# Optimization experiments

Measured on AMD Instinct MI355X. Metric: run time of the kernel, lower is better.

The kernel has to match this reference:

```python
import jax, jax.numpy as jnp
import numpy as np

NUM_HEADS = 16
HEAD_DIM = 64
LN_EPS = 1e-12


def _interleave_pairs(a, b):
    # stack([a, b], -1).reshape(..., 2*d) -> interleaved on last dim
    return jnp.stack([a, b], axis=-1).reshape(a.shape[:-1] + (a.shape[-1] * 2,))


def _rotate_half(x):
    # stack([-x[..., 1::2], x[..., ::2]], -1).reshape_as(x)
    return _interleave_pairs(-x[..., 1::2], x[..., ::2])


def setup_inputs() -> dict:
    key = jax.random.key(0)
    ks = jax.random.split(key, 4)
    B, S, H = 4, 2048, 1024
    hidden_states = jax.random.normal(ks[0], (B, S, H), dtype=jnp.float32)
    sinusoidal_pos = jax.random.uniform(ks[1], (1, 1, S, HEAD_DIM), dtype=jnp.float32)
    ln_weight = jnp.ones((H,), dtype=jnp.float32)
    ln_bias = jnp.zeros((H,), dtype=jnp.float32)
    w_qkv = jax.random.normal(ks[2], (H, 3 * H), dtype=jnp.float32) * (1.0 / np.sqrt(H))
    b_qkv = jax.random.normal(ks[3], (3 * H,), dtype=jnp.float32) * 0.02
    return {"hidden_states": hidden_states, "sinusoidal_pos": sinusoidal_pos,
            "ln_weight": ln_weight, "ln_bias": ln_bias, "w_qkv": w_qkv, "b_qkv": b_qkv}


def reference(hidden_states, sinusoidal_pos, ln_weight, ln_bias, w_qkv, b_qkv):
    B, S, H = hidden_states.shape
    # LayerNorm
    mu = jnp.mean(hidden_states, axis=-1, keepdims=True)
    var = jnp.mean(jnp.square(hidden_states - mu), axis=-1, keepdims=True)
    h = (hidden_states - mu) * jax.lax.rsqrt(var + LN_EPS) * ln_weight + ln_bias
    # Fused QKV projection
    qkv = h @ w_qkv + b_qkv                       # [B, S, 3H]
    q, k, v = jnp.split(qkv, 3, axis=-1)
    def to_heads(x):
        return x.reshape(B, S, NUM_HEADS, HEAD_DIM).transpose(0, 2, 1, 3)  # [B, Hn, S, D]
    q, k, v = to_heads(q), to_heads(k), to_heads(v)
    # RoPE (RoFormer interleaved style)
    sin, cos = jnp.split(sinusoidal_pos, 2, axis=-1)      # each [1,1,S,D/2]
    sin_pos = _interleave_pairs(sin, sin)                 # [1,1,S,D]
    cos_pos = _interleave_pairs(cos, cos)
    q = q * cos_pos + _rotate_half(q) * sin_pos
    k = k * cos_pos + _rotate_half(k) * sin_pos
    # SDPA (non-causal, no mask, eval-mode dropout=0)
    scale = 1.0 / np.sqrt(HEAD_DIM)
    scores = jnp.einsum('bhqd,bhkd->bhqk', q, k) * scale
    probs = jax.nn.softmax(scores, axis=-1)
    ctx = jnp.einsum('bhqk,bhkd->bhqd', probs, v)         # [B, Hn, S, D]
    ctx = ctx.transpose(0, 2, 1, 3).reshape(B, S, H)
    return ctx
```

## Files before the change

kernel.cpp:

```cpp
#include <hip/hip_runtime.h>
#include <hip/hip_bf16.h>
#include <cstdint>
#include <cstddef>

#define DEVINL __device__ __forceinline__

typedef float f32x4 __attribute__((ext_vector_type(4)));
typedef float f32x16 __attribute__((ext_vector_type(16)));
typedef short s16x8 __attribute__((ext_vector_type(8)));
typedef short s16x4 __attribute__((ext_vector_type(4)));

static constexpr int Sd = 2048;
static constexpr int Hd = 1024;
static constexpr int NHd = 16;
static constexpr int Dd = 64;
static constexpr int N3 = 3072;

DEVINL float bf2f(short u){
  unsigned int t = ((unsigned int)(unsigned short)u) << 16;
  float f; __builtin_memcpy(&f, &t, 4); return f;
}
DEVINL short f2bf(float f){
  unsigned int t; __builtin_memcpy(&t, &f, 4);
  unsigned int r = t + 0x7FFFu + ((t >> 16) & 1u);
  return (short)(r >> 16);
}

DEVINL void gld16(const short* g, short* l){
  __builtin_amdgcn_global_load_lds((const __attribute__((address_space(1))) unsigned int*)g,
                                   (__attribute__((address_space(3))) unsigned int*)l, 16, 0, 0);
}

DEVINL int cvtpk(float lo, float hi){
  int r; asm("v_cvt_pk_bf16_f32 %0, %1, %2" : "=v"(r) : "v"(lo), "v"(hi)); return r;
}

DEVINL float fexp2(float x){
#if __has_builtin(__builtin_amdgcn_exp2f)
  return __builtin_amdgcn_exp2f(x);
#else
  return exp2f(x);
#endif
}

DEVINL f32x16 z16(){
  f32x16 v;
  #pragma unroll
  for (int i=0;i<16;i++) v[i]=0.f;
  return v;
}

__global__ __launch_bounds__(256) void ln_kernel(const float* __restrict__ x,
                                                 const float* __restrict__ w,
                                                 const float* __restrict__ bs,
                                                 short* __restrict__ h){
  int row = blockIdx.x, tid = threadIdx.x;
  const float* xr = x + (size_t)row * Hd;
  f32x4 v = *(const f32x4*)(xr + tid*4);
  float s1 = v[0]+v[1]+v[2]+v[3];
  float s2 = v[0]*v[0]+v[1]*v[1]+v[2]*v[2]+v[3]*v[3];
  #pragma unroll
  for (int off = 1; off < 64; off <<= 1){ s1 += __shfl_xor(s1, off); s2 += __shfl_xor(s2, off); }
  __shared__ float red[8];
  if ((tid & 63) == 0){ red[(tid>>6)*2] = s1; red[(tid>>6)*2+1] = s2; }
  __syncthreads();
  s1 = red[0]+red[2]+red[4]+red[6];
  s2 = red[1]+red[3]+red[5]+red[7];
  float mu = s1 * (1.0f/Hd);
  float rstd = rsqrtf(s2*(1.0f/Hd) - mu*mu + 1e-12f);
  f32x4 wv = *(const f32x4*)(w + tid*4);
  f32x4 bv = *(const f32x4*)(bs + tid*4);
  s16x4 o;
  #pragma unroll
  for (int i=0;i<4;i++) o[i] = f2bf((v[i]-mu)*rstd*wv[i] + bv[i]);
  *(s16x4*)(h + (size_t)row*Hd + tid*4) = o;
}

__global__ __launch_bounds__(256) void castw_kernel(const float* __restrict__ w, short* __restrict__ wT){
  __shared__ float t[32][33];
  int n0 = blockIdx.x*32, k0 = blockIdx.y*32;
  int tx = threadIdx.x, ty = threadIdx.y;
  #pragma unroll
  for (int i=0;i<4;i++) t[ty + i*8][tx] = w[(size_t)(k0 + ty + i*8)*N3 + n0 + tx];
  __syncthreads();
  #pragma unroll
  for (int i=0;i<4;i++) wT[(size_t)(n0 + ty + i*8)*Hd + k0 + tx] = f2bf(t[tx][ty + i*8]);
}

__global__ __launch_bounds__(256) void gemm_kernel(const short* __restrict__ A,
                                                   const short* __restrict__ Bt,
                                                   const float* __restrict__ bias,
                                                   short* __restrict__ qo,
                                                   short* __restrict__ ko,
                                                   short* __restrict__ vo){
  __shared__ short lA[128*32];
  __shared__ short lB[128*32];
  int bid = blockIdx.x;
  int xcd = bid & 7, idx = bid >> 3;
  int mt = xcd*8 + (idx & 7), nt = idx >> 3;
  int m0 = mt*128, n0 = nt*128;
  int tid = threadIdx.x, lane = tid & 63, wv = tid >> 6;
  int l15 = lane & 15, lq = lane >> 4;
  int wr = wv >> 1, wc = wv & 1;
  f32x4 zero = {0.f,0.f,0.f,0.f};
  f32x4 acc[4][4];
  #pragma unroll
  for (int m=0;m<4;m++)
    #pragma unroll
    for (int n=0;n<4;n++) acc[m][n] = zero;
  int flat = tid*8;
  int row0 = flat >> 5, col0 = flat & 31;
  const short* ga = A  + (size_t)(m0 + row0)*Hd + col0;
  const short* gb = Bt + (size_t)(n0 + row0)*Hd + col0;
  short* lAw = lA + wv*512;
  short* lBw = lB + wv*512;
  for (int kk = 0; kk < Hd; kk += 32){
    __syncthreads();
    gld16(ga + kk,                 lAw);
    gld16(ga + kk + (size_t)64*Hd, lAw + 2048);
    gld16(gb + kk,                 lBw);
    gld16(gb + kk + (size_t)64*Hd, lBw + 2048);
    __syncthreads();
    s16x8 af[4], bf[4];
    #pragma unroll
    for (int m=0;m<4;m++) af[m] = *(const s16x8*)(lA + (wr*64 + m*16 + l15)*32 + 8*lq);
    #pragma unroll
    for (int n=0;n<4;n++) bf[n] = *(const s16x8*)(lB + (wc*64 + n*16 + l15)*32 + 8*lq);
    #pragma unroll
    for (int m=0;m<4;m++)
      #pragma unroll
      for (int n=0;n<4;n++)
        acc[m][n] = __builtin_amdgcn_mfma_f32_16x16x32_bf16(af[m], bf[n], acc[m][n], 0, 0, 0);
  }
  #pragma unroll
  for (int n=0;n<4;n++){
    int c = n0 + wc*64 + n*16 + l15;
    float bv = bias[c];
    int part = c >> 10, hh = (c >> 6) & 15, d = c & 63;
    short* dst = part == 0 ? qo : (part == 1 ? ko : vo);
    #pragma unroll
    for (int m=0;m<4;m++){
      #pragma unroll
      for (int j=0;j<4;j++){
        int r = m0 + wr*64 + m*16 + lq*4 + j;
        int b = r >> 11, s = r & 2047;
        dst[(((size_t)((b*NHd + hh)*Sd + s)) << 6) + d] = f2bf(acc[m][n][j] + bv);
      }
    }
  }
}

__global__ __launch_bounds__(256) void rope_kernel(short* __restrict__ q, short* __restrict__ k,
                                                   const float* __restrict__ sp){
  unsigned int idx = blockIdx.x*256 + threadIdx.x;
  int part = idx >> 19;
  unsigned int r = (idx >> 2) & 131071u;
  int quarter = idx & 3;
  int s = r & 2047;
  short* p = (part ? k : q) + ((size_t)r << 6) + quarter*16;
  s16x8 x0 = *(s16x8*)(p), x1 = *(s16x8*)(p + 8);
  const float* sr = sp + (size_t)s*64 + quarter*8;
  f32x4 sn0 = *(const f32x4*)(sr),      sn1 = *(const f32x4*)(sr + 4);
  f32x4 cs0 = *(const f32x4*)(sr + 32), cs1 = *(const f32x4*)(sr + 36);
  float scale = part ? 1.0f : 0.18033688011112042f;
  s16x8 y0, y1;
  #pragma unroll
  for (int j=0;j<4;j++){
    float e = bf2f(x0[2*j]), o = bf2f(x0[2*j+1]);
    y0[2*j]   = f2bf((e*cs0[j] - o*sn0[j])*scale);
    y0[2*j+1] = f2bf((o*cs0[j] + e*sn0[j])*scale);
    float e1 = bf2f(x1[2*j]), o1 = bf2f(x1[2*j+1]);
    y1[2*j]   = f2bf((e1*cs1[j] - o1*sn1[j])*scale);
    y1[2*j+1] = f2bf((o1*cs1[j] + e1*sn1[j])*scale);
  }
  *(s16x8*)(p) = y0; *(s16x8*)(p + 8) = y1;
}

__global__ __launch_bounds__(256) void vt_kernel(const short* __restrict__ v, short* __restrict__ vT){
  __shared__ short t[64*65];
  int s0 = blockIdx.x*64, bh = blockIdx.y;
  int tid = threadIdx.x;
  int srow = tid >> 2, cb = (tid & 3) * 16;
  const short* src = v + (((size_t)bh*Sd + s0 + srow) << 6) + cb;
  s16x8 a = *(const s16x8*)(src), b = *(const s16x8*)(src + 8);
  #pragma unroll
  for (int j=0;j<8;j++){ t[(cb+j)*65 + srow] = a[j]; t[(cb+8+j)*65 + srow] = b[j]; }
  __syncthreads();
  int d = tid >> 2, sb = (tid & 3) * 16;
  s16x8 o0, o1;
  #pragma unroll
  for (int j=0;j<8;j++){ o0[j] = t[d*65 + sb + j]; o1[j] = t[d*65 + sb + 8 + j]; }
  size_t obase = (((size_t)bh*Dd + d) << 11) + s0 + sb;
  *(s16x8*)(vT + obase)     = o0;
  *(s16x8*)(vT + obase + 8) = o1;
}

__global__ __launch_bounds__(512, 4) void attn_kernel(const short* __restrict__ q,
                                                      const short* __restrict__ k,
                                                      const short* __restrict__ vT,
                                                      float* __restrict__ out){
  __shared__ alignas(16) short kbuf[2][4096];
  __shared__ alignas(16) short vbuf[2][4096];
  int bid = blockIdx.x;
  int xcd = bid & 7, w = bid >> 3;
  int bh = xcd*8 + (w >> 3), qb = w & 7;
  int tid = threadIdx.x, lane = tid & 63, wv = tid >> 6;
  int l31 = lane & 31, hi = lane >> 5;
  const short* kp = k  + ((size_t)bh << 17);
  const short* vp = vT + ((size_t)bh << 17);
  int qrow = qb*256 + wv*32 + l31;
  const short* qp = q + ((size_t)bh << 17) + (size_t)qrow*64;
  s16x8 qf[4];
  #pragma unroll
  for (int kk=0;kk<4;kk++) qf[kk] = *(const s16x8*)(qp + kk*16 + hi*8);

  int crow = tid >> 3;
  int scol = ((tid & 7) ^ (crow & 7)) * 8;
  const short* kg = kp + crow*64 + scol;
  const short* vg = vp + (size_t)crow*2048 + scol;

  f32x16 ot0 = z16(), ot1 = z16();
  float m = -1e30f, lr = 0.f;
  int rsw = (l31 & 7);

  gld16(kg, &kbuf[0][0] + wv*512);
  gld16(vg, &vbuf[0][0] + wv*512);
  __syncthreads();

  for (int t = 0; t < 32; ++t){
    int cur = t & 1;
    if (t < 31){
      gld16(kg + (t+1)*4096, &kbuf[cur^1][0] + wv*512);
      gld16(vg + (t+1)*64,   &vbuf[cur^1][0] + wv*512);
    }
    const short* kb = &kbuf[cur][0];
    const short* vb = &vbuf[cur][0];
    f32x16 s0 = z16(), s1 = z16();
    #pragma unroll
    for (int kk=0;kk<4;kk++){
      s16x8 kf0 = *(const s16x8*)(kb + l31*64       + (((kk*2 + hi) ^ rsw)*8));
      s0 = __builtin_amdgcn_mfma_f32_32x32x16_bf16(kf0, qf[kk], s0, 0, 0, 0);
      s16x8 kf1 = *(const s16x8*)(kb + (32+l31)*64  + (((kk*2 + hi) ^ rsw)*8));
      s1 = __builtin_amdgcn_mfma_f32_32x32x16_bf16(kf1, qf[kk], s1, 0, 0, 0);
    }
    float tm[16];
    #pragma unroll
    for (int i=0;i<16;i++) tm[i] = fmaxf(s0[i], s1[i]);
    #pragma unroll
    for (int off=8; off>=1; off>>=1)
      #pragma unroll
      for (int i=0;i<off;i++) tm[i] = fmaxf(tm[i], tm[i+off]);
    float pmax = fmaxf(tm[0], __shfl_xor(tm[0], 32));
    if (!__all(pmax - m <= 8.0f)){
      float mn = fmaxf(m, pmax);
      float al = fexp2(m - mn);
      m = mn; lr *= al;
      #pragma unroll
      for (int i=0;i<16;i++){ ot0[i] *= al; ot1[i] *= al; }
    }
    float rs = 0.f;
    #pragma unroll
    for (int i=0;i<16;i++){ s0[i] = fexp2(s0[i]-m); s1[i] = fexp2(s1[i]-m); }
    #pragma unroll
    for (int i=0;i<16;i++) rs += s0[i] + s1[i];
    lr += rs + __shfl_xor(rs, 32);
    #pragma unroll
    for (int s4=0;s4<4;s4++){
      int base = (s4 & 1) * 8;
      int pkA0, pkA1, pkB0, pkB1;
      if (s4 < 2){
        pkA0 = cvtpk(s0[base],   s0[base+1]); pkA1 = cvtpk(s0[base+2], s0[base+3]);
        pkB0 = cvtpk(s0[base+4], s0[base+5]); pkB1 = cvtpk(s0[base+6], s0[base+7]);
      } else {
        pkA0 = cvtpk(s1[base],   s1[base+1]); pkA1 = cvtpk(s1[base+2], s1[base+3]);
        pkB0 = cvtpk(s1[base+4], s1[base+5]); pkB1 = cvtpk(s1[base+6], s1[base+7]);
      }
      int r0 = __shfl_xor(hi ? pkA0 : pkB0, 32);
      int r1 = __shfl_xor(hi ? pkA1 : pkB1, 32);
      union { int wq[4]; s16x8 v8; } u;
      u.wq[0] = hi ? r0   : pkA0;
      u.wq[1] = hi ? r1   : pkA1;
      u.wq[2] = hi ? pkB0 : r0;
      u.wq[3] = hi ? pkB1 : r1;
      s16x8 vf0 = *(const s16x8*)(vb + l31*64      + (((s4*2 + hi) ^ rsw)*8));
      ot0 = __builtin_amdgcn_mfma_f32_32x32x16_bf16(vf0, u.v8, ot0, 0, 0, 0);
      s16x8 vf1 = *(const s16x8*)(vb + (32+l31)*64 + (((s4*2 + hi) ^ rsw)*8));
      ot1 = __builtin_amdgcn_mfma_f32_32x32x16_bf16(vf1, u.v8, ot1, 0, 0, 0);
    }
    __syncthreads();
  }
  float inv = 1.0f / lr;
  int b = bh >> 4, hh = bh & 15;
  float* orow = out + ((size_t)(b*Sd + qrow) << 10) + hh*64;
  #pragma unroll
  for (int g=0; g<4; ++g){
    f32x4 w0, w1;
    #pragma unroll
    for (int j=0;j<4;j++){ w0[j] = ot0[4*g+j]*inv; w1[j] = ot1[4*g+j]*inv; }
    *(f32x4*)(orow + g*8 + 4*hi)      = w0;
    *(f32x4*)(orow + 32 + g*8 + 4*hi) = w1;
  }
}

extern "C" void kernel_launch(void* const* d_in, const int* in_sizes, int n_in,
                              void* d_out, int out_size, void* d_ws, size_t ws_size,
                              hipStream_t stream){
  const float* hs = (const float*)d_in[0];
  const float* sp = (const float*)d_in[1];
  const float* lw = (const float*)d_in[2];
  const float* lb = (const float*)d_in[3];
  const float* wq = (const float*)d_in[4];
  const float* bq = (const float*)d_in[5];
  float* out = (float*)d_out;
  char* ws = (char*)d_ws;
  short* h   = (short*)(ws);
  short* wT  = (short*)(ws + 16777216);
  short* vTb = (short*)(ws);
  short* qb_ = (short*)(ws + 23068672);
  short* kb_ = (short*)(ws + 23068672 + 16777216);
  short* vb_ = (short*)(ws + 23068672 + 33554432);

  hipLaunchKernelGGL(ln_kernel,    dim3(8192),   dim3(256),   0, stream, hs, lw, lb, h);
  hipLaunchKernelGGL(castw_kernel, dim3(96,32),  dim3(32,8),  0, stream, wq, wT);
  hipLaunchKernelGGL(gemm_kernel,  dim3(1536),   dim3(256),   0, stream, h, wT, bq, qb_, kb_, vb_);
  hipLaunchKernelGGL(rope_kernel,  dim3(4096),   dim3(256),   0, stream, qb_, kb_, sp);
  hipLaunchKernelGGL(vt_kernel,    dim3(32,64),  dim3(256),   0, stream, vb_, vTb);
  hipLaunchKernelGGL(attn_kernel,  dim3(512),    dim3(512),   0, stream, qb_, kb_, vTb, out);
}
```

Baseline: 194.0 us.

## Fuse Q RoPE into attention, merge K RoPE with V transpose, double KV tile

Measured after the change: 185.5 us. 4.4% less time.

```diff
diff --git a/kernel.cpp b/kernel.cpp
--- a/kernel.cpp
+++ b/kernel.cpp
@@ -150,57 +150,58 @@
   }
 }
 
-__global__ __launch_bounds__(256) void rope_kernel(short* __restrict__ q, short* __restrict__ k,
+__global__ __launch_bounds__(256) void prep_kernel(short* __restrict__ k,
+                                                   const short* __restrict__ v,
+                                                   short* __restrict__ vT,
                                                    const float* __restrict__ sp){
-  unsigned int idx = blockIdx.x*256 + threadIdx.x;
-  int part = idx >> 19;
-  unsigned int r = (idx >> 2) & 131071u;
-  int quarter = idx & 3;
-  int s = r & 2047;
-  short* p = (part ? k : q) + ((size_t)r << 6) + quarter*16;
-  s16x8 x0 = *(s16x8*)(p), x1 = *(s16x8*)(p + 8);
-  const float* sr = sp + (size_t)s*64 + quarter*8;
-  f32x4 sn0 = *(const f32x4*)(sr),      sn1 = *(const f32x4*)(sr + 4);
-  f32x4 cs0 = *(const f32x4*)(sr + 32), cs1 = *(const f32x4*)(sr + 36);
-  float scale = part ? 1.0f : 0.18033688011112042f;
-  s16x8 y0, y1;
-  #pragma unroll
-  for (int j=0;j<4;j++){
-    float e = bf2f(x0[2*j]), o = bf2f(x0[2*j+1]);
-    y0[2*j]   = f2bf((e*cs0[j] - o*sn0[j])*scale);
-    y0[2*j+1] = f2bf((o*cs0[j] + e*sn0[j])*scale);
-    float e1 = bf2f(x1[2*j]), o1 = bf2f(x1[2*j+1]);
-    y1[2*j]   = f2bf((e1*cs1[j] - o1*sn1[j])*scale);
-    y1[2*j+1] = f2bf((o1*cs1[j] + e1*sn1[j])*scale);
-  }
-  *(s16x8*)(p) = y0; *(s16x8*)(p + 8) = y1;
-}
-
-__global__ __launch_bounds__(256) void vt_kernel(const short* __restrict__ v, short* __restrict__ vT){
-  __shared__ short t[64*65];
-  int s0 = blockIdx.x*64, bh = blockIdx.y;
-  int tid = threadIdx.x;
-  int srow = tid >> 2, cb = (tid & 3) * 16;
-  const short* src = v + (((size_t)bh*Sd + s0 + srow) << 6) + cb;
-  s16x8 a = *(const s16x8*)(src), b = *(const s16x8*)(src + 8);
-  #pragma unroll
-  for (int j=0;j<8;j++){ t[(cb+j)*65 + srow] = a[j]; t[(cb+8+j)*65 + srow] = b[j]; }
-  __syncthreads();
-  int d = tid >> 2, sb = (tid & 3) * 16;
-  s16x8 o0, o1;
-  #pragma unroll
-  for (int j=0;j<8;j++){ o0[j] = t[d*65 + sb + j]; o1[j] = t[d*65 + sb + 8 + j]; }
-  size_t obase = (((size_t)bh*Dd + d) << 11) + s0 + sb;
-  *(s16x8*)(vT + obase)     = o0;
-  *(s16x8*)(vT + obase + 8) = o1;
+  if (blockIdx.y == 0){
+    unsigned int idx = blockIdx.x*256 + threadIdx.x;
+    unsigned int r = idx >> 2;
+    int quarter = idx & 3;
+    int s = r & 2047;
+    short* p = k + ((size_t)r << 6) + quarter*16;
+    s16x8 x0 = *(s16x8*)(p), x1 = *(s16x8*)(p + 8);
+    const float* sr = sp + (size_t)s*64 + quarter*8;
+    f32x4 sn0 = *(const f32x4*)(sr),      sn1 = *(const f32x4*)(sr + 4);
+    f32x4 cs0 = *(const f32x4*)(sr + 32), cs1 = *(const f32x4*)(sr + 36);
+    s16x8 y0, y1;
+    #pragma unroll
+    for (int j=0;j<4;j++){
+      float e = bf2f(x0[2*j]), o = bf2f(x0[2*j+1]);
+      y0[2*j]   = f2bf(e*cs0[j] - o*sn0[j]);
+      y0[2*j+1] = f2bf(o*cs0[j] + e*sn0[j]);
+      float e1 = bf2f(x1[2*j]), o1 = bf2f(x1[2*j+1]);
+      y1[2*j]   = f2bf(e1*cs1[j] - o1*sn1[j]);
+      y1[2*j+1] = f2bf(o1*cs1[j] + e1*sn1[j]);
+    }
+    *(s16x8*)(p) = y0; *(s16x8*)(p + 8) = y1;
+  } else {
+    __shared__ short t[64*65];
+    int s0 = (blockIdx.x & 31)*64, bh = blockIdx.x >> 5;
+    int tid = threadIdx.x;
+    int srow = tid >> 2, cb = (tid & 3) * 16;
+    const short* src = v + (((size_t)bh*Sd + s0 + srow) << 6) + cb;
+    s16x8 a = *(const s16x8*)(src), b = *(const s16x8*)(src + 8);
+    #pragma unroll
+    for (int j=0;j<8;j++){ t[(cb+j)*65 + srow] = a[j]; t[(cb+8+j)*65 + srow] = b[j]; }
+    __syncthreads();
+    int d = tid >> 2, sb = (tid & 3) * 16;
+    s16x8 o0, o1;
+    #pragma unroll
+    for (int j=0;j<8;j++){ o0[j] = t[d*65 + sb + j]; o1[j] = t[d*65 + sb + 8 + j]; }
+    size_t obase = (((size_t)bh*Dd + d) << 11) + s0 + sb;
+    *(s16x8*)(vT + obase)     = o0;
+    *(s16x8*)(vT + obase + 8) = o1;
+  }
 }
 
 __global__ __launch_bounds__(512, 4) void attn_kernel(const short* __restrict__ q,
                                                       const short* __restrict__ k,
                                                       const short* __restrict__ vT,
+                                                      const float* __restrict__ sp,
                                                       float* __restrict__ out){
-  __shared__ alignas(16) short kbuf[2][4096];
-  __shared__ alignas(16) short vbuf[2][4096];
+  __shared__ alignas(16) short kbuf[2][8192];
+  __shared__ alignas(16) short vbuf[2][8192];
   int bid = blockIdx.x;
   int xcd = bid & 7, w = bid >> 3;
   int bh = xcd*8 + (w >> 3), qb = w & 7;
@@ -210,85 +211,117 @@
   const short* vp = vT + ((size_t)bh << 17);
   int qrow = qb*256 + wv*32 + l31;
   const short* qp = q + ((size_t)bh << 17) + (size_t)qrow*64;
+  const float* spq = sp + (size_t)qrow*64;
+  const float qs = 0.18033688011112042f;
   s16x8 qf[4];
   #pragma unroll
-  for (int kk=0;kk<4;kk++) qf[kk] = *(const s16x8*)(qp + kk*16 + hi*8);
-
-  int crow = tid >> 3;
-  int scol = ((tid & 7) ^ (crow & 7)) * 8;
-  const short* kg = kp + crow*64 + scol;
-  const short* vg = vp + (size_t)crow*2048 + scol;
+  for (int kk=0;kk<4;kk++){
+    s16x8 x = *(const s16x8*)(qp + kk*16 + hi*8);
+    f32x4 sn = *(const f32x4*)(spq + kk*8 + hi*4);
+    f32x4 cs = *(const f32x4*)(spq + 32 + kk*8 + hi*4);
+    s16x8 y;
+    #pragma unroll
+    for (int j=0;j<4;j++){
+      float e = bf2f(x[2*j]), o = bf2f(x[2*j+1]);
+      y[2*j]   = f2bf((e*cs[j] - o*sn[j])*qs);
+      y[2*j+1] = f2bf((o*cs[j] + e*sn[j])*qs);
+    }
+    qf[kk] = y;
+  }
+  int kc0 = tid,      kr0 = kc0 >> 3;
+  int kc1 = tid+512,  kr1 = kc1 >> 3;
+  int koff0 = kr0*64 + ((kc0 ^ kr0) & 7)*8;
+  int koff1 = kr1*64 + ((kc1 ^ kr1) & 7)*8;
+  int vr0 = tid >> 4,       vcc0 = tid & 15;
+  int vr1 = (tid+512) >> 4, vcc1 = (tid+512) & 15;
+  int voff0 = vr0*2048 + ((vcc0 & 8) | ((vcc0 ^ vr0) & 7))*8;
+  int voff1 = vr1*2048 + ((vcc1 & 8) | ((vcc1 ^ vr1) & 7))*8;
 
   f32x16 ot0 = z16(), ot1 = z16();
   float m = -1e30f, lr = 0.f;
   int rsw = (l31 & 7);
 
-  gld16(kg, &kbuf[0][0] + wv*512);
-  gld16(vg, &vbuf[0][0] + wv*512);
+#define STAGE(nb, t) do { \
+    gld16(kp + (size_t)(t)*8192 + koff0, &kbuf[nb][0]    + wv*512); \
+    gld16(kp + (size_t)(t)*8192 + koff1, &kbuf[nb][4096] + wv*512); \
+    gld16(vp + (size_t)(t)*128  + voff0, &vbuf[nb][0]    + wv*512); \
+    gld16(vp + (size_t)(t)*128  + voff1, &vbuf[nb][4096] + wv*512); \
+  } while(0)
+
+  STAGE(0, 0);
   __syncthreads();
 
-  for (int t = 0; t < 32; ++t){
+  for (int t = 0; t < 16; ++t){
     int cur = t & 1;
-    if (t < 31){
-      gld16(kg + (t+1)*4096, &kbuf[cur^1][0] + wv*512);
-      gld16(vg + (t+1)*64,   &vbuf[cur^1][0] + wv*512);
-    }
-    const short* kb = &kbuf[cur][0];
-    const short* vb = &vbuf[cur][0];
-    f32x16 s0 = z16(), s1 = z16();
-    #pragma unroll
-    for (int kk=0;kk<4;kk++){
-      s16x8 kf0 = *(const s16x8*)(kb + l31*64       + (((kk*2 + hi) ^ rsw)*8));
-      s0 = __builtin_amdgcn_mfma_f32_32x32x16_bf16(kf0, qf[kk], s0, 0, 0, 0);
-      s16x8 kf1 = *(const s16x8*)(kb + (32+l31)*64  + (((kk*2 + hi) ^ rsw)*8));
-      s1 = __builtin_amdgcn_mfma_f32_32x32x16_bf16(kf1, qf[kk], s1, 0, 0, 0);
-    }
-    float tm[16];
-    #pragma unroll
-    for (int i=0;i<16;i++) tm[i] = fmaxf(s0[i], s1[i]);
-    #pragma unroll
-    for (int off=8; off>=1; off>>=1)
-      #pragma unroll
-      for (int i=0;i<off;i++) tm[i] = fmaxf(tm[i], tm[i+off]);
-    float pmax = fmaxf(tm[0], __shfl_xor(tm[0], 32));
-    if (!__all(pmax - m <= 8.0f)){
-      float mn = fmaxf(m, pmax);
-      float al = fexp2(m - mn);
-      m = mn; lr *= al;
-      #pragma unroll
-      for (int i=0;i<16;i++){ ot0[i] *= al; ot1[i] *= al; }
-    }
-    float rs = 0.f;
-    #pragma unroll
-    for (int i=0;i<16;i++){ s0[i] = fexp2(s0[i]-m); s1[i] = fexp2(s1[i]-m); }
-    #pragma unroll
-    for (int i=0;i<16;i++) rs += s0[i] + s1[i];
-    lr += rs + __shfl_xor(rs, 32);
-    #pragma unroll
-    for (int s4=0;s4<4;s4++){
-      int base = (s4 & 1) * 8;
-      int pkA0, pkA1, pkB0, pkB1;
-      if (s4 < 2){
-        pkA0 = cvtpk(s0[base],   s0[base+1]); pkA1 = cvtpk(s0[base+2], s0[base+3]);
-        pkB0 = cvtpk(s0[base+4], s0[base+5]); pkB1 = cvtpk(s0[base+6], s0[base+7]);
-      } else {
-        pkA0 = cvtpk(s1[base],   s1[base+1]); pkA1 = cvtpk(s1[base+2], s1[base+3]);
-        pkB0 = cvtpk(s1[base+4], s1[base+5]); pkB1 = cvtpk(s1[base+6], s1[base+7]);
+    if (t < 15) STAGE(cur^1, t+1);
+    #pragma unroll
+    for (int h = 0; h < 2; ++h){
+      const short* kb = &kbuf[cur][h*4096];
+      const short* vb = &vbuf[cur][h*64];
+      f32x16 s0 = z16(), s1 = z16();
+      __builtin_amdgcn_s_setprio(1);
+      #pragma unroll
+      for (int kk=0;kk<4;kk++){
+        s16x8 kf0 = *(const s16x8*)(kb + l31*64       + (((kk*2 + hi) ^ rsw)*8));
+        s0 = __builtin_amdgcn_mfma_f32_32x32x16_bf16(kf0, qf[kk], s0, 0, 0, 0);
+        s16x8 kf1 = *(const s16x8*)(kb + (32+l31)*64  + (((kk*2 + hi) ^ rsw)*8));
+        s1 = __builtin_amdgcn_mfma_f32_32x32x16_bf16(kf1, qf[kk], s1, 0, 0, 0);
       }
-      int r0 = __shfl_xor(hi ? pkA0 : pkB0, 32);
-      int r1 = __shfl_xor(hi ? pkA1 : pkB1, 32);
-      union { int wq[4]; s16x8 v8; } u;
-      u.wq[0] = hi ? r0   : pkA0;
-      u.wq[1] = hi ? r1   : pkA1;
-      u.wq[2] = hi ? pkB0 : r0;
-      u.wq[3] = hi ? pkB1 : r1;
-      s16x8 vf0 = *(const s16x8*)(vb + l31*64      + (((s4*2 + hi) ^ rsw)*8));
-      ot0 = __builtin_amdgcn_mfma_f32_32x32x16_bf16(vf0, u.v8, ot0, 0, 0, 0);
-      s16x8 vf1 = *(const s16x8*)(vb + (32+l31)*64 + (((s4*2 + hi) ^ rsw)*8));
-      ot1 = __builtin_amdgcn_mfma_f32_32x32x16_bf16(vf1, u.v8, ot1, 0, 0, 0);
+      __builtin_amdgcn_s_setprio(0);
+      float tm[16];
+      #pragma unroll
+      for (int i=0;i<16;i++) tm[i] = fmaxf(s0[i], s1[i]);
+      #pragma unroll
+      for (int off=8; off>=1; off>>=1)
+        #pragma unroll
+        for (int i=0;i<off;i++) tm[i] = fmaxf(tm[i], tm[i+off]);
+      float pmax = fmaxf(tm[0], __shfl_xor(tm[0], 32));
+      if (!__all(pmax - m <= 8.0f)){
+        float mn = fmaxf(m, pmax);
+        float al = fexp2(m - mn);
+        m = mn; lr *= al;
+        #pragma unroll
+        for (int i=0;i<16;i++){ ot0[i] *= al; ot1[i] *= al; }
+      }
+      #pragma unroll
+      for (int i=0;i<16;i++){ s0[i] = fexp2(s0[i]-m); s1[i] = fexp2(s1[i]-m); }
+      float ra[16];
+      #pragma unroll
+      for (int i=0;i<16;i++) ra[i] = s0[i] + s1[i];
+      #pragma unroll
+      for (int off=8; off>=1; off>>=1)
+        #pragma unroll
+        for (int i=0;i<off;i++) ra[i] += ra[i+off];
+      lr += ra[0] + __shfl_xor(ra[0], 32);
+      #pragma unroll
+      for (int s4=0;s4<4;s4++){
+        int base = (s4 & 1) * 8;
+        int pkA0, pkA1, pkB0, pkB1;
+        if (s4 < 2){
+          pkA0 = cvtpk(s0[base],   s0[base+1]); pkA1 = cvtpk(s0[base+2], s0[base+3]);
+          pkB0 = cvtpk(s0[base+4], s0[base+5]); pkB1 = cvtpk(s0[base+6], s0[base+7]);
+        } else {
+          pkA0 = cvtpk(s1[base],   s1[base+1]); pkA1 = cvtpk(s1[base+2], s1[base+3]);
+          pkB0 = cvtpk(s1[base+4], s1[base+5]); pkB1 = cvtpk(s1[base+6], s1[base+7]);
+        }
+        int r0 = __shfl_xor(hi ? pkA0 : pkB0, 32);
+        int r1 = __shfl_xor(hi ? pkA1 : pkB1, 32);
+        union { int wq[4]; s16x8 v8; } u;
+        u.wq[0] = hi ? r0   : pkA0;
+        u.wq[1] = hi ? r1   : pkA1;
+        u.wq[2] = hi ? pkB0 : r0;
+        u.wq[3] = hi ? pkB1 : r1;
+        __builtin_amdgcn_s_setprio(1);
+        s16x8 vf0 = *(const s16x8*)(vb + l31*128      + (((s4*2 + hi) ^ rsw)*8));
+        ot0 = __builtin_amdgcn_mfma_f32_32x32x16_bf16(vf0, u.v8, ot0, 0, 0, 0);
+        s16x8 vf1 = *(const s16x8*)(vb + (32+l31)*128 + (((s4*2 + hi) ^ rsw)*8));
+        ot1 = __builtin_amdgcn_mfma_f32_32x32x16_bf16(vf1, u.v8, ot1, 0, 0, 0);
+        __builtin_amdgcn_s_setprio(0);
+      }
     }
     __syncthreads();
   }
+#undef STAGE
   float inv = 1.0f / lr;
   int b = bh >> 4, hh = bh & 15;
   float* orow = out + ((size_t)(b*Sd + qrow) << 10) + hh*64;
@@ -320,10 +353,9 @@
   short* kb_ = (short*)(ws + 23068672 + 16777216);
   short* vb_ = (short*)(ws + 23068672 + 33554432);
 
-  hipLaunchKernelGGL(ln_kernel,    dim3(8192),   dim3(256),   0, stream, hs, lw, lb, h);
-  hipLaunchKernelGGL(castw_kernel, dim3(96,32),  dim3(32,8),  0, stream, wq, wT);
-  hipLaunchKernelGGL(gemm_kernel,  dim3(1536),   dim3(256),   0, stream, h, wT, bq, qb_, kb_, vb_);
-  hipLaunchKernelGGL(rope_kernel,  dim3(4096),   dim3(256),   0, stream, qb_, kb_, sp);
-  hipLaunchKernelGGL(vt_kernel,    dim3(32,64),  dim3(256),   0, stream, vb_, vTb);
-  hipLaunchKernelGGL(attn_kernel,  dim3(512),    dim3(512),   0, stream, qb_, kb_, vTb, out);
-}
+  hipLaunchKernelGGL(ln_kernel,    dim3(8192),    dim3(256),   0, stream, hs, lw, lb, h);
+  hipLaunchKernelGGL(castw_kernel, dim3(96,32),   dim3(32,8),  0, stream, wq, wT);
+  hipLaunchKernelGGL(gemm_kernel,  dim3(1536),    dim3(256),   0, stream, h, wT, bq, qb_, kb_, vb_);
+  hipLaunchKernelGGL(prep_kernel,  dim3(2048,2),  dim3(256),   0, stream, kb_, vb_, vTb, sp);
+  hipLaunchKernelGGL(attn_kernel,  dim3(512),     dim3(512),   0, stream, qb_, kb_, vTb, sp, out);
+}
```
